# Performance work log

Hardware: AMD Instinct MI355X
Metric: run time of the kernel (lower is better)

## Reference

```python
import jax, jax.numpy as jnp
import numpy as np

EPS = 1e-5
SINKHORN_ITERS = 20
ALPHA_INIT = 0.01


def setup_inputs() -> dict:
    key = jax.random.key(0)
    ks = jax.random.split(key, 8)
    B, n, C = 8192, 4, 2048
    nC = n * C
    return {
        "x_expanded": jax.random.normal(ks[0], (B, n, C), dtype=jnp.float32),
        "rmsnorm_weight": jnp.ones((C,), dtype=jnp.float32),
        "phi_pre": 0.02 * jax.random.normal(ks[1], (n, nC), dtype=jnp.float32),
        "phi_post": 0.02 * jax.random.normal(ks[2], (n, nC), dtype=jnp.float32),
        "phi_res": 0.02 * jax.random.normal(ks[3], (n * n, nC), dtype=jnp.float32),
        "b_pre": jnp.zeros((n,), dtype=jnp.float32),
        "b_post": jnp.zeros((n,), dtype=jnp.float32),
        "b_res": jnp.zeros((n, n), dtype=jnp.float32),
        "alpha_pre": jnp.float32(ALPHA_INIT),
        "alpha_post": jnp.float32(ALPHA_INIT),
        "alpha_res": jnp.float32(ALPHA_INIT),
    }


def _rmsnorm(x, w, eps):
    # RMSNorm over the channel dim C of each stream
    ms = jnp.mean(x * x, axis=-1, keepdims=True)
    return x * jax.lax.rsqrt(ms + eps) * w


def _sinkhorn(logits, iters, eps):
    # logits: (B, n, n) -> doubly-stochastic matrix via Sinkhorn-Knopp
    m = jnp.exp(logits - jnp.max(logits, axis=(1, 2), keepdims=True))
    for _ in range(iters):
        m = m / (jnp.sum(m, axis=2, keepdims=True) + eps)  # row normalize
        m = m / (jnp.sum(m, axis=1, keepdims=True) + eps)  # col normalize
    return m


def reference(x_expanded, rmsnorm_weight, phi_pre, phi_post, phi_res,
              b_pre, b_post, b_res, alpha_pre, alpha_post, alpha_res):
    B, n, C = x_expanded.shape
    x_norm = _rmsnorm(x_expanded, rmsnorm_weight, EPS)   # (B, n, C)
    xf = x_norm.reshape(B, n * C)                         # (B, nC)

    # dynamic mixing coefficients from learned projections
    h_pre = alpha_pre * (xf @ phi_pre.T) + b_pre          # (B, n)
    h_post = alpha_post * (xf @ phi_post.T) + b_post      # (B, n)
    h_res_logits = (alpha_res * (xf @ phi_res.T) + b_res.reshape(-1)).reshape(B, n, n)

    h_res = _sinkhorn(h_res_logits, SINKHORN_ITERS, EPS)  # (B, n, n) doubly stochastic

    # blended mixing of the raw residual streams
    mixed = jnp.einsum('bij,bjc->bic', h_res, x_expanded)        # (B, n, C)
    agg = jnp.einsum('bn,bnc->bc', h_pre, x_expanded)            # (B, C)
    out = mixed + h_post[:, :, None] * agg[:, None, :]           # (B, n, C)
    return out
```

## Files before the change

kernel.cpp:

```cpp
#include <hip/hip_runtime.h>
#include <hip/hip_bf16.h>
#include <cstdint>

#define CH 2048
#define NCF 8192
#define NJ 24
#define RPB 4
#define EPS_F 1e-5f
#define SINK_ITERS 20

typedef float v4f __attribute__((ext_vector_type(4)));

__device__ __forceinline__ uint32_t bf16rne(float f) {
    uint32_t u = __float_as_uint(f);
    return (u + 0x7fffu + ((u >> 16) & 1u)) >> 16;
}

__device__ __forceinline__ float dot8(const uint4& x, const uint4& p, float acc) {
    asm("v_dot2_f32_bf16 %0, %1, %2, %0" : "+v"(acc) : "v"(x.x), "v"(p.x));
    asm("v_dot2_f32_bf16 %0, %1, %2, %0" : "+v"(acc) : "v"(x.y), "v"(p.y));
    asm("v_dot2_f32_bf16 %0, %1, %2, %0" : "+v"(acc) : "v"(x.z), "v"(p.z));
    asm("v_dot2_f32_bf16 %0, %1, %2, %0" : "+v"(acc) : "v"(x.w), "v"(p.w));
    return acc;
}

__global__ void __launch_bounds__(256) prep_phi_kernel(
    const float* __restrict__ w,
    const float* __restrict__ phi_pre,
    const float* __restrict__ phi_post,
    const float* __restrict__ phi_res,
    const float* __restrict__ alpha_pre,
    const float* __restrict__ alpha_post,
    const float* __restrict__ alpha_res,
    uint16_t* __restrict__ phiW)
{
    int idx = blockIdx.x * 256 + threadIdx.x;
    if (idx >= NJ * NCF) return;
    int j = idx / NCF;
    int k = idx - j * NCF;
    int c = k & (CH - 1);
    float v, a;
    if (j < 4)      { v = phi_pre[j * NCF + k];        a = alpha_pre[0]; }
    else if (j < 8) { v = phi_post[(j - 4) * NCF + k]; a = alpha_post[0]; }
    else            { v = phi_res[(j - 8) * NCF + k];  a = alpha_res[0]; }
    phiW[idx] = (uint16_t)bf16rne(v * a * w[c]);
}

__global__ void __launch_bounds__(512) mhc_main_kernel(
    const float* __restrict__ x,
    const uint16_t* __restrict__ phiW,
    const float* __restrict__ b_pre,
    const float* __restrict__ b_post,
    const float* __restrict__ b_res,
    float* __restrict__ out)
{
    const int t = threadIdx.x;
    const int lane = t & 63;
    const int wave = t >> 6;
    const long b0 = (long)blockIdx.x * RPB;

    __shared__ uint32_t xn[RPB][NCF / 2];
    __shared__ float4 red[RPB][8];
    __shared__ float H[RPB][24] __attribute__((aligned(16)));
    __shared__ float MS[RPB][16] __attribute__((aligned(16)));

    {
        const float4* xp = reinterpret_cast<const float4*>(x + b0 * NCF);
        #pragma unroll
        for (int rp = 0; rp < RPB; rp += 2) {
            float4 a[2][4];
            #pragma unroll
            for (int rr = 0; rr < 2; ++rr)
                #pragma unroll
                for (int jj = 0; jj < 4; ++jj)
                    a[rr][jj] = xp[(rp + rr) * 2048 + t + 512 * jj];

            float ss[2][4];
            #pragma unroll
            for (int rr = 0; rr < 2; ++rr) {
                const int r = rp + rr;
                #pragma unroll
                for (int jj = 0; jj < 4; ++jj) {
                    float4 v = a[rr][jj];
                    ss[rr][jj] = v.x*v.x + v.y*v.y + v.z*v.z + v.w*v.w;
                    *reinterpret_cast<uint2*>(&xn[r][2*t + 1024*jj]) =
                        make_uint2(bf16rne(v.x) | (bf16rne(v.y) << 16),
                                   bf16rne(v.z) | (bf16rne(v.w) << 16));
                }
            }
            #pragma unroll
            for (int m = 1; m < 64; m <<= 1) {
                #pragma unroll
                for (int rr = 0; rr < 2; ++rr)
                    #pragma unroll
                    for (int jj = 0; jj < 4; ++jj)
                        ss[rr][jj] += __shfl_xor(ss[rr][jj], m, 64);
            }
            if (lane == 0) {
                red[rp][wave]     = make_float4(ss[0][0], ss[0][1], ss[0][2], ss[0][3]);
                red[rp + 1][wave] = make_float4(ss[1][0], ss[1][1], ss[1][2], ss[1][3]);
            }
        }
    }
    __syncthreads();

    float scl[RPB][4];
    #pragma unroll
    for (int r = 0; r < RPB; ++r) {
        float sx = 0.f, sy = 0.f, sz = 0.f, sw = 0.f;
        #pragma unroll
        for (int w8 = 0; w8 < 8; ++w8) {
            float4 v = red[r][w8];
            sx += v.x; sy += v.y; sz += v.z; sw += v.w;
        }
        scl[r][0] = rsqrtf(sx * (1.0f / CH) + EPS_F);
        scl[r][1] = rsqrtf(sy * (1.0f / CH) + EPS_F);
        scl[r][2] = rsqrtf(sz * (1.0f / CH) + EPS_F);
        scl[r][3] = rsqrtf(sw * (1.0f / CH) + EPS_F);
    }

    float accT[3][RPB] = {};
    float accS[3][RPB] = {};
    {
        const uint16_t* pw = phiW + (size_t)(wave * 3) * NCF;
        const int kl = 8 * lane;
        const uint4* xr0 = reinterpret_cast<const uint4*>(xn[0]);
        const uint4* xr1 = reinterpret_cast<const uint4*>(xn[1]);
        const uint4* xr2 = reinterpret_cast<const uint4*>(xn[2]);
        const uint4* xr3 = reinterpret_cast<const uint4*>(xn[3]);

        uint4 pA0 = *reinterpret_cast<const uint4*>(pw + 0 * NCF + kl);
        uint4 pA1 = *reinterpret_cast<const uint4*>(pw + 1 * NCF + kl);
        uint4 pA2 = *reinterpret_cast<const uint4*>(pw + 2 * NCF + kl);
        uint4 xA0 = xr0[lane], xA1 = xr1[lane], xA2 = xr2[lane], xA3 = xr3[lane];

        #pragma unroll
        for (int u = 0; u < 16; u += 2) {
            const int iB = 64 * (u + 1) + lane;
            const int kB = 512 * (u + 1) + kl;
            uint4 pB0 = *reinterpret_cast<const uint4*>(pw + 0 * NCF + kB);
            uint4 pB1 = *reinterpret_cast<const uint4*>(pw + 1 * NCF + kB);
            uint4 pB2 = *reinterpret_cast<const uint4*>(pw + 2 * NCF + kB);
            uint4 xB0 = xr0[iB], xB1 = xr1[iB], xB2 = xr2[iB], xB3 = xr3[iB];

            accS[0][0] = dot8(xA0, pA0, accS[0][0]);
            accS[0][1] = dot8(xA1, pA0, accS[0][1]);
            accS[0][2] = dot8(xA2, pA0, accS[0][2]);
            accS[0][3] = dot8(xA3, pA0, accS[0][3]);
            accS[1][0] = dot8(xA0, pA1, accS[1][0]);
            accS[1][1] = dot8(xA1, pA1, accS[1][1]);
            accS[1][2] = dot8(xA2, pA1, accS[1][2]);
            accS[1][3] = dot8(xA3, pA1, accS[1][3]);
            accS[2][0] = dot8(xA0, pA2, accS[2][0]);
            accS[2][1] = dot8(xA1, pA2, accS[2][1]);
            accS[2][2] = dot8(xA2, pA2, accS[2][2]);
            accS[2][3] = dot8(xA3, pA2, accS[2][3]);

            if (u + 2 < 16) {
                const int iA = 64 * (u + 2) + lane;
                const int kA = 512 * (u + 2) + kl;
                pA0 = *reinterpret_cast<const uint4*>(pw + 0 * NCF + kA);
                pA1 = *reinterpret_cast<const uint4*>(pw + 1 * NCF + kA);
                pA2 = *reinterpret_cast<const uint4*>(pw + 2 * NCF + kA);
                xA0 = xr0[iA]; xA1 = xr1[iA]; xA2 = xr2[iA]; xA3 = xr3[iA];
            }

            accS[0][0] = dot8(xB0, pB0, accS[0][0]);
            accS[0][1] = dot8(xB1, pB0, accS[0][1]);
            accS[0][2] = dot8(xB2, pB0, accS[0][2]);
            accS[0][3] = dot8(xB3, pB0, accS[0][3]);
            accS[1][0] = dot8(xB0, pB1, accS[1][0]);
            accS[1][1] = dot8(xB1, pB1, accS[1][1]);
            accS[1][2] = dot8(xB2, pB1, accS[1][2]);
            accS[1][3] = dot8(xB3, pB1, accS[1][3]);
            accS[2][0] = dot8(xB0, pB2, accS[2][0]);
            accS[2][1] = dot8(xB1, pB2, accS[2][1]);
            accS[2][2] = dot8(xB2, pB2, accS[2][2]);
            accS[2][3] = dot8(xB3, pB2, accS[2][3]);

            if (((u + 1) & 3) == 3) {
                const int s = (u + 1) >> 2;
                #pragma unroll
                for (int jl = 0; jl < 3; ++jl) {
                    #pragma unroll
                    for (int r = 0; r < RPB; ++r) {
                        accT[jl][r] = fmaf(scl[r][s], accS[jl][r], accT[jl][r]);
                        accS[jl][r] = 0.f;
                    }
                }
            }
        }
    }
    {
        #pragma unroll
        for (int m = 1; m < 64; m <<= 1) {
            #pragma unroll
            for (int jl = 0; jl < 3; ++jl) {
                #pragma unroll
                for (int r = 0; r < RPB; ++r)
                    accT[jl][r] += __shfl_xor(accT[jl][r], m, 64);
            }
        }
        if (lane == 0) {
            #pragma unroll
            for (int jl = 0; jl < 3; ++jl) {
                int j = 3 * wave + jl;
                float bias;
                if (j < 4)      bias = b_pre[j];
                else if (j < 8) bias = b_post[j - 4];
                else            bias = b_res[j - 8];
                #pragma unroll
                for (int r = 0; r < RPB; ++r) H[r][j] = accT[jl][r] + bias;
            }
        }
    }
    __syncthreads();

    {
        const int r = lane >> 4;
        const int q = lane & 15;
        float L = H[r][8 + q];
        float mx = L;
        mx = fmaxf(mx, __shfl_xor(mx, 1, 64));
        mx = fmaxf(mx, __shfl_xor(mx, 2, 64));
        mx = fmaxf(mx, __shfl_xor(mx, 4, 64));
        mx = fmaxf(mx, __shfl_xor(mx, 8, 64));
        float m = __expf(L - mx);
        #pragma unroll
        for (int it = 0; it < SINK_ITERS; ++it) {
            float rs = m + __shfl_xor(m, 1, 64);
            rs += __shfl_xor(rs, 2, 64);
            m = m * __builtin_amdgcn_rcpf(rs + EPS_F);
            float cs = m + __shfl_xor(m, 4, 64);
            cs += __shfl_xor(cs, 8, 64);
            m = m * __builtin_amdgcn_rcpf(cs + EPS_F);
        }
        MS[r][q] = m;
    }

    #pragma unroll
    for (int r = 0; r < RPB; ++r) {
        const float4 hp = *reinterpret_cast<const float4*>(&H[r][0]);
        const float4 hq = *reinterpret_cast<const float4*>(&H[r][4]);
        float4 hrm[4];
        #pragma unroll
        for (int i = 0; i < 4; ++i)
            hrm[i] = *reinterpret_cast<const float4*>(&MS[r][4 * i]);
        float4 s[4];
        #pragma unroll
        for (int jj = 0; jj < 4; ++jj) {
            uint2 pk = *reinterpret_cast<const uint2*>(&xn[r][2 * t + 1024 * jj]);
            s[jj].x = __uint_as_float(pk.x << 16);
            s[jj].y = __uint_as_float(pk.x & 0xffff0000u);
            s[jj].z = __uint_as_float(pk.y << 16);
            s[jj].w = __uint_as_float(pk.y & 0xffff0000u);
        }
        float ax = hp.x*s[0].x + hp.y*s[1].x + hp.z*s[2].x + hp.w*s[3].x;
        float ay = hp.x*s[0].y + hp.y*s[1].y + hp.z*s[2].y + hp.w*s[3].y;
        float az = hp.x*s[0].z + hp.y*s[1].z + hp.z*s[2].z + hp.w*s[3].z;
        float aw = hp.x*s[0].w + hp.y*s[1].w + hp.z*s[2].w + hp.w*s[3].w;
        const float hqv[4] = {hq.x, hq.y, hq.z, hq.w};
        v4f* op = reinterpret_cast<v4f*>(out + (b0 + r) * NCF + 4 * t);
        #pragma unroll
        for (int i = 0; i < 4; ++i) {
            v4f o;
            o.x = hrm[i].x*s[0].x + hrm[i].y*s[1].x + hrm[i].z*s[2].x + hrm[i].w*s[3].x + hqv[i]*ax;
            o.y = hrm[i].x*s[0].y + hrm[i].y*s[1].y + hrm[i].z*s[2].y + hrm[i].w*s[3].y + hqv[i]*ay;
            o.z = hrm[i].x*s[0].z + hrm[i].y*s[1].z + hrm[i].z*s[2].z + hrm[i].w*s[3].z + hqv[i]*az;
            o.w = hrm[i].x*s[0].w + hrm[i].y*s[1].w + hrm[i].z*s[2].w + hrm[i].w*s[3].w + hqv[i]*aw;
            __builtin_nontemporal_store(o, op + i * 512);
        }
    }
}

extern "C" void kernel_launch(void* const* d_in, const int* in_sizes, int n_in,
                              void* d_out, int out_size, void* d_ws, size_t ws_size,
                              hipStream_t stream)
{
    const float* x        = (const float*)d_in[0];
    const float* w        = (const float*)d_in[1];
    const float* phi_pre  = (const float*)d_in[2];
    const float* phi_post = (const float*)d_in[3];
    const float* phi_res  = (const float*)d_in[4];
    const float* b_pre    = (const float*)d_in[5];
    const float* b_post   = (const float*)d_in[6];
    const float* b_res    = (const float*)d_in[7];
    const float* a_pre    = (const float*)d_in[8];
    const float* a_post   = (const float*)d_in[9];
    const float* a_res    = (const float*)d_in[10];
    float* out = (float*)d_out;
    uint16_t* phiW = (uint16_t*)d_ws;

    const int B = in_sizes[0] / NCF;

    prep_phi_kernel<<<(NJ * NCF + 255) / 256, 256, 0, stream>>>(
        w, phi_pre, phi_post, phi_res, a_pre, a_post, a_res, phiW);

    mhc_main_kernel<<<B / RPB, 512, 0, stream>>>(
        x, phiW, b_pre, b_post, b_res, out);
}
```

Before: 133.1 us.

## Split fused kernel into coefficient kernel and fp32 mixing kernel

```diff
diff --git a/kernel.cpp b/kernel.cpp
--- a/kernel.cpp
+++ b/kernel.cpp
@@ -14,6 +14,12 @@
 __device__ __forceinline__ uint32_t bf16rne(float f) {
     uint32_t u = __float_as_uint(f);
     return (u + 0x7fffu + ((u >> 16) & 1u)) >> 16;
+}
+
+__device__ __forceinline__ uint32_t cvtpk(float lo, float hi) {
+    uint32_t r;
+    asm("v_cvt_pk_bf16_f32 %0, %1, %2" : "=v"(r) : "v"(lo), "v"(hi));
+    return r;
 }
 
 __device__ __forceinline__ float dot8(const uint4& x, const uint4& p, float acc) {
@@ -46,13 +52,13 @@
     phiW[idx] = (uint16_t)bf16rne(v * a * w[c]);
 }
 
-__global__ void __launch_bounds__(512) mhc_main_kernel(
+__global__ void __launch_bounds__(512) h_kernel(
     const float* __restrict__ x,
     const uint16_t* __restrict__ phiW,
     const float* __restrict__ b_pre,
     const float* __restrict__ b_post,
     const float* __restrict__ b_res,
-    float* __restrict__ out)
+    float* __restrict__ hbuf)
 {
     const int t = threadIdx.x;
     const int lane = t & 63;
@@ -84,8 +90,7 @@
                     float4 v = a[rr][jj];
                     ss[rr][jj] = v.x*v.x + v.y*v.y + v.z*v.z + v.w*v.w;
                     *reinterpret_cast<uint2*>(&xn[r][2*t + 1024*jj]) =
-                        make_uint2(bf16rne(v.x) | (bf16rne(v.y) << 16),
-                                   bf16rne(v.z) | (bf16rne(v.w) << 16));
+                        make_uint2(cvtpk(v.x, v.y), cvtpk(v.z, v.w));
                 }
             }
             #pragma unroll
@@ -238,38 +243,67 @@
         MS[r][q] = m;
     }
 
-    #pragma unroll
-    for (int r = 0; r < RPB; ++r) {
-        const float4 hp = *reinterpret_cast<const float4*>(&H[r][0]);
-        const float4 hq = *reinterpret_cast<const float4*>(&H[r][4]);
-        float4 hrm[4];
-        #pragma unroll
-        for (int i = 0; i < 4; ++i)
-            hrm[i] = *reinterpret_cast<const float4*>(&MS[r][4 * i]);
-        float4 s[4];
-        #pragma unroll
-        for (int jj = 0; jj < 4; ++jj) {
-            uint2 pk = *reinterpret_cast<const uint2*>(&xn[r][2 * t + 1024 * jj]);
-            s[jj].x = __uint_as_float(pk.x << 16);
-            s[jj].y = __uint_as_float(pk.x & 0xffff0000u);
-            s[jj].z = __uint_as_float(pk.y << 16);
-            s[jj].w = __uint_as_float(pk.y & 0xffff0000u);
-        }
-        float ax = hp.x*s[0].x + hp.y*s[1].x + hp.z*s[2].x + hp.w*s[3].x;
-        float ay = hp.x*s[0].y + hp.y*s[1].y + hp.z*s[2].y + hp.w*s[3].y;
-        float az = hp.x*s[0].z + hp.y*s[1].z + hp.z*s[2].z + hp.w*s[3].z;
-        float aw = hp.x*s[0].w + hp.y*s[1].w + hp.z*s[2].w + hp.w*s[3].w;
-        const float hqv[4] = {hq.x, hq.y, hq.z, hq.w};
-        v4f* op = reinterpret_cast<v4f*>(out + (b0 + r) * NCF + 4 * t);
-        #pragma unroll
-        for (int i = 0; i < 4; ++i) {
-            v4f o;
-            o.x = hrm[i].x*s[0].x + hrm[i].y*s[1].x + hrm[i].z*s[2].x + hrm[i].w*s[3].x + hqv[i]*ax;
-            o.y = hrm[i].x*s[0].y + hrm[i].y*s[1].y + hrm[i].z*s[2].y + hrm[i].w*s[3].y + hqv[i]*ay;
-            o.z = hrm[i].x*s[0].z + hrm[i].y*s[1].z + hrm[i].z*s[2].z + hrm[i].w*s[3].z + hqv[i]*az;
-            o.w = hrm[i].x*s[0].w + hrm[i].y*s[1].w + hrm[i].z*s[2].w + hrm[i].w*s[3].w + hqv[i]*aw;
-            __builtin_nontemporal_store(o, op + i * 512);
-        }
+    if (t < 96) {
+        const int r = t / 24;
+        const int k = t - 24 * r;
+        float v = (k < 8) ? H[r][k] : MS[r][k - 8];
+        hbuf[(b0 + r) * 24 + k] = v;
+    }
+}
+
+__global__ void __launch_bounds__(512) mix_kernel(
+    const float* __restrict__ x,
+    const float* __restrict__ hbuf,
+    float* __restrict__ out)
+{
+    const int t = threadIdx.x;
+    const long b = blockIdx.x;
+
+    const float4* hb = reinterpret_cast<const float4*>(hbuf + b * 24);
+    const float4 hp = hb[0];
+    const float4 hq = hb[1];
+    const float4 h0 = hb[2], h1 = hb[3], h2 = hb[4], h3 = hb[5];
+
+    const float4* xp = reinterpret_cast<const float4*>(x + b * NCF) + t;
+    const float4 s0 = xp[0], s1 = xp[512], s2 = xp[1024], s3 = xp[1536];
+
+    const float ax = hp.x*s0.x + hp.y*s1.x + hp.z*s2.x + hp.w*s3.x;
+    const float ay = hp.x*s0.y + hp.y*s1.y + hp.z*s2.y + hp.w*s3.y;
+    const float az = hp.x*s0.z + hp.y*s1.z + hp.z*s2.z + hp.w*s3.z;
+    const float aw = hp.x*s0.w + hp.y*s1.w + hp.z*s2.w + hp.w*s3.w;
+
+    v4f* op = reinterpret_cast<v4f*>(out + b * NCF) + t;
+    {
+        v4f o;
+        o.x = h0.x*s0.x + h0.y*s1.x + h0.z*s2.x + h0.w*s3.x + hq.x*ax;
+        o.y = h0.x*s0.y + h0.y*s1.y + h0.z*s2.y + h0.w*s3.y + hq.x*ay;
+        o.z = h0.x*s0.z + h0.y*s1.z + h0.z*s2.z + h0.w*s3.z + hq.x*az;
+        o.w = h0.x*s0.w + h0.y*s1.w + h0.z*s2.w + h0.w*s3.w + hq.x*aw;
+        __builtin_nontemporal_store(o, op);
+    }
+    {
+        v4f o;
+        o.x = h1.x*s0.x + h1.y*s1.x + h1.z*s2.x + h1.w*s3.x + hq.y*ax;
+        o.y = h1.x*s0.y + h1.y*s1.y + h1.z*s2.y + h1.w*s3.y + hq.y*ay;
+        o.z = h1.x*s0.z + h1.y*s1.z + h1.z*s2.z + h1.w*s3.z + hq.y*az;
+        o.w = h1.x*s0.w + h1.y*s1.w + h1.z*s2.w + h1.w*s3.w + hq.y*aw;
+        __builtin_nontemporal_store(o, op + 512);
+    }
+    {
+        v4f o;
+        o.x = h2.x*s0.x + h2.y*s1.x + h2.z*s2.x + h2.w*s3.x + hq.z*ax;
+        o.y = h2.x*s0.y + h2.y*s1.y + h2.z*s2.y + h2.w*s3.y + hq.z*ay;
+        o.z = h2.x*s0.z + h2.y*s1.z + h2.z*s2.z + h2.w*s3.z + hq.z*az;
+        o.w = h2.x*s0.w + h2.y*s1.w + h2.z*s2.w + h2.w*s3.w + hq.z*aw;
+        __builtin_nontemporal_store(o, op + 1024);
+    }
+    {
+        v4f o;
+        o.x = h3.x*s0.x + h3.y*s1.x + h3.z*s2.x + h3.w*s3.x + hq.w*ax;
+        o.y = h3.x*s0.y + h3.y*s1.y + h3.z*s2.y + h3.w*s3.y + hq.w*ay;
+        o.z = h3.x*s0.z + h3.y*s1.z + h3.z*s2.z + h3.w*s3.z + hq.w*az;
+        o.w = h3.x*s0.w + h3.y*s1.w + h3.z*s2.w + h3.w*s3.w + hq.w*aw;
+        __builtin_nontemporal_store(o, op + 1536);
     }
 }
 
@@ -289,13 +323,17 @@
     const float* a_post   = (const float*)d_in[9];
     const float* a_res    = (const float*)d_in[10];
     float* out = (float*)d_out;
+
     uint16_t* phiW = (uint16_t*)d_ws;
+    float* hbuf = (float*)((char*)d_ws + (size_t)NJ * NCF * 2);
 
     const int B = in_sizes[0] / NCF;
 
     prep_phi_kernel<<<(NJ * NCF + 255) / 256, 256, 0, stream>>>(
         w, phi_pre, phi_post, phi_res, a_pre, a_post, a_res, phiW);
 
-    mhc_main_kernel<<<B / RPB, 512, 0, stream>>>(
-        x, phiW, b_pre, b_post, b_res, out);
-}
+    h_kernel<<<B / RPB, 512, 0, stream>>>(
+        x, phiW, b_pre, b_post, b_res, hbuf);
+
+    mix_kernel<<<B, 512, 0, stream>>>(x, hbuf, out);
+}
```

Result: slower. 172.0 us (+29.2%).

## Make main kernel persistent with register prefetch of next row group

Applied to the files above, without the earlier changes.

```diff
diff --git a/kernel.cpp b/kernel.cpp
--- a/kernel.cpp
+++ b/kernel.cpp
@@ -6,6 +6,7 @@
 #define NCF 8192
 #define NJ 24
 #define RPB 4
+#define NBLK 512
 #define EPS_F 1e-5f
 #define SINK_ITERS 20
 
@@ -14,6 +15,12 @@
 __device__ __forceinline__ uint32_t bf16rne(float f) {
     uint32_t u = __float_as_uint(f);
     return (u + 0x7fffu + ((u >> 16) & 1u)) >> 16;
+}
+
+__device__ __forceinline__ uint32_t cvtpk(float lo, float hi) {
+    uint32_t r;
+    asm("v_cvt_pk_bf16_f32 %0, %1, %2" : "=v"(r) : "v"(lo), "v"(hi));
+    return r;
 }
 
 __device__ __forceinline__ float dot8(const uint4& x, const uint4& p, float acc) {
@@ -46,230 +53,244 @@
     phiW[idx] = (uint16_t)bf16rne(v * a * w[c]);
 }
 
-__global__ void __launch_bounds__(512) mhc_main_kernel(
+__global__ void __launch_bounds__(512, 2) mhc_main_kernel(
     const float* __restrict__ x,
     const uint16_t* __restrict__ phiW,
     const float* __restrict__ b_pre,
     const float* __restrict__ b_post,
     const float* __restrict__ b_res,
-    float* __restrict__ out)
+    float* __restrict__ out,
+    int ngroups)
 {
     const int t = threadIdx.x;
     const int lane = t & 63;
     const int wave = t >> 6;
-    const long b0 = (long)blockIdx.x * RPB;
 
     __shared__ uint32_t xn[RPB][NCF / 2];
     __shared__ float4 red[RPB][8];
     __shared__ float H[RPB][24] __attribute__((aligned(16)));
     __shared__ float MS[RPB][16] __attribute__((aligned(16)));
 
+    float bias[3];
+    #pragma unroll
+    for (int jl = 0; jl < 3; ++jl) {
+        int j = 3 * wave + jl;
+        bias[jl] = (j < 4) ? b_pre[j] : (j < 8) ? b_post[j - 4] : b_res[j - 8];
+    }
+
+    const float4* x4 = reinterpret_cast<const float4*>(x);
+
+    float4 xr[16];
     {
-        const float4* xp = reinterpret_cast<const float4*>(x + b0 * NCF);
+        const float4* xp = x4 + (long)blockIdx.x * RPB * 2048;
         #pragma unroll
-        for (int rp = 0; rp < RPB; rp += 2) {
-            float4 a[2][4];
-            #pragma unroll
-            for (int rr = 0; rr < 2; ++rr)
-                #pragma unroll
-                for (int jj = 0; jj < 4; ++jj)
-                    a[rr][jj] = xp[(rp + rr) * 2048 + t + 512 * jj];
-
-            float ss[2][4];
-            #pragma unroll
-            for (int rr = 0; rr < 2; ++rr) {
-                const int r = rp + rr;
+        for (int r = 0; r < RPB; ++r)
+            #pragma unroll
+            for (int jj = 0; jj < 4; ++jj)
+                xr[r * 4 + jj] = xp[r * 2048 + t + 512 * jj];
+    }
+
+    #pragma unroll 1
+    for (long g = blockIdx.x; g < ngroups; g += NBLK) {
+        const long b0 = g * RPB;
+
+        {
+            float ssv[16];
+            #pragma unroll
+            for (int r = 0; r < RPB; ++r) {
                 #pragma unroll
                 for (int jj = 0; jj < 4; ++jj) {
-                    float4 v = a[rr][jj];
-                    ss[rr][jj] = v.x*v.x + v.y*v.y + v.z*v.z + v.w*v.w;
+                    float4 v = xr[r * 4 + jj];
+                    ssv[r * 4 + jj] = v.x*v.x + v.y*v.y + v.z*v.z + v.w*v.w;
                     *reinterpret_cast<uint2*>(&xn[r][2*t + 1024*jj]) =
-                        make_uint2(bf16rne(v.x) | (bf16rne(v.y) << 16),
-                                   bf16rne(v.z) | (bf16rne(v.w) << 16));
+                        make_uint2(cvtpk(v.x, v.y), cvtpk(v.z, v.w));
                 }
             }
             #pragma unroll
-            for (int m = 1; m < 64; m <<= 1) {
-                #pragma unroll
-                for (int rr = 0; rr < 2; ++rr)
+            for (int m = 1; m < 64; m <<= 1)
+                #pragma unroll
+                for (int i = 0; i < 16; ++i)
+                    ssv[i] += __shfl_xor(ssv[i], m, 64);
+            if (lane == 0) {
+                #pragma unroll
+                for (int r = 0; r < RPB; ++r)
+                    red[r][wave] = make_float4(ssv[r*4], ssv[r*4+1], ssv[r*4+2], ssv[r*4+3]);
+            }
+        }
+        __syncthreads();
+
+        float scl[RPB][4];
+        #pragma unroll
+        for (int r = 0; r < RPB; ++r) {
+            float sx = 0.f, sy = 0.f, sz = 0.f, sw = 0.f;
+            #pragma unroll
+            for (int w8 = 0; w8 < 8; ++w8) {
+                float4 v = red[r][w8];
+                sx += v.x; sy += v.y; sz += v.z; sw += v.w;
+            }
+            scl[r][0] = rsqrtf(sx * (1.0f / CH) + EPS_F);
+            scl[r][1] = rsqrtf(sy * (1.0f / CH) + EPS_F);
+            scl[r][2] = rsqrtf(sz * (1.0f / CH) + EPS_F);
+            scl[r][3] = rsqrtf(sw * (1.0f / CH) + EPS_F);
+        }
+
+        float accT[3][RPB] = {};
+        float accS[3][RPB] = {};
+        {
+            const uint16_t* pw = phiW + (size_t)(wave * 3) * NCF;
+            const int kl = 8 * lane;
+            const uint4* xr0 = reinterpret_cast<const uint4*>(xn[0]);
+            const uint4* xr1 = reinterpret_cast<const uint4*>(xn[1]);
+            const uint4* xr2 = reinterpret_cast<const uint4*>(xn[2]);
+            const uint4* xr3 = reinterpret_cast<const uint4*>(xn[3]);
+
+            uint4 pA0 = *reinterpret_cast<const uint4*>(pw + 0 * NCF + kl);
+            uint4 pA1 = *reinterpret_cast<const uint4*>(pw + 1 * NCF + kl);
+            uint4 pA2 = *reinterpret_cast<const uint4*>(pw + 2 * NCF + kl);
+            uint4 xA0 = xr0[lane], xA1 = xr1[lane], xA2 = xr2[lane], xA3 = xr3[lane];
+
+            #pragma unroll
+            for (int u = 0; u < 16; u += 2) {
+                const int iB = 64 * (u + 1) + lane;
+                const int kB = 512 * (u + 1) + kl;
+                uint4 pB0 = *reinterpret_cast<const uint4*>(pw + 0 * NCF + kB);
+                uint4 pB1 = *reinterpret_cast<const uint4*>(pw + 1 * NCF + kB);
+                uint4 pB2 = *reinterpret_cast<const uint4*>(pw + 2 * NCF + kB);
+                uint4 xB0 = xr0[iB], xB1 = xr1[iB], xB2 = xr2[iB], xB3 = xr3[iB];
+
+                accS[0][0] = dot8(xA0, pA0, accS[0][0]);
+                accS[0][1] = dot8(xA1, pA0, accS[0][1]);
+                accS[0][2] = dot8(xA2, pA0, accS[0][2]);
+                accS[0][3] = dot8(xA3, pA0, accS[0][3]);
+                accS[1][0] = dot8(xA0, pA1, accS[1][0]);
+                accS[1][1] = dot8(xA1, pA1, accS[1][1]);
+                accS[1][2] = dot8(xA2, pA1, accS[1][2]);
+                accS[1][3] = dot8(xA3, pA1, accS[1][3]);
+                accS[2][0] = dot8(xA0, pA2, accS[2][0]);
+                accS[2][1] = dot8(xA1, pA2, accS[2][1]);
+                accS[2][2] = dot8(xA2, pA2, accS[2][2]);
+                accS[2][3] = dot8(xA3, pA2, accS[2][3]);
+
+                if (u + 2 < 16) {
+                    const int iA = 64 * (u + 2) + lane;
+                    const int kA = 512 * (u + 2) + kl;
+                    pA0 = *reinterpret_cast<const uint4*>(pw + 0 * NCF + kA);
+                    pA1 = *reinterpret_cast<const uint4*>(pw + 1 * NCF + kA);
+                    pA2 = *reinterpret_cast<const uint4*>(pw + 2 * NCF + kA);
+                    xA0 = xr0[iA]; xA1 = xr1[iA]; xA2 = xr2[iA]; xA3 = xr3[iA];
+                }
+
+                accS[0][0] = dot8(xB0, pB0, accS[0][0]);
+                accS[0][1] = dot8(xB1, pB0, accS[0][1]);
+                accS[0][2] = dot8(xB2, pB0, accS[0][2]);
+                accS[0][3] = dot8(xB3, pB0, accS[0][3]);
+                accS[1][0] = dot8(xB0, pB1, accS[1][0]);
+                accS[1][1] = dot8(xB1, pB1, accS[1][1]);
+                accS[1][2] = dot8(xB2, pB1, accS[1][2]);
+                accS[1][3] = dot8(xB3, pB1, accS[1][3]);
+                accS[2][0] = dot8(xB0, pB2, accS[2][0]);
+                accS[2][1] = dot8(xB1, pB2, accS[2][1]);
+                accS[2][2] = dot8(xB2, pB2, accS[2][2]);
+                accS[2][3] = dot8(xB3, pB2, accS[2][3]);
+
+                if (((u + 1) & 3) == 3) {
+                    const int s = (u + 1) >> 2;
                     #pragma unroll
-                    for (int jj = 0; jj < 4; ++jj)
-                        ss[rr][jj] += __shfl_xor(ss[rr][jj], m, 64);
-            }
-            if (lane == 0) {
-                red[rp][wave]     = make_float4(ss[0][0], ss[0][1], ss[0][2], ss[0][3]);
-                red[rp + 1][wave] = make_float4(ss[1][0], ss[1][1], ss[1][2], ss[1][3]);
-            }
-        }
-    }
-    __syncthreads();
-
-    float scl[RPB][4];
-    #pragma unroll
-    for (int r = 0; r < RPB; ++r) {
-        float sx = 0.f, sy = 0.f, sz = 0.f, sw = 0.f;
-        #pragma unroll
-        for (int w8 = 0; w8 < 8; ++w8) {
-            float4 v = red[r][w8];
-            sx += v.x; sy += v.y; sz += v.z; sw += v.w;
-        }
-        scl[r][0] = rsqrtf(sx * (1.0f / CH) + EPS_F);
-        scl[r][1] = rsqrtf(sy * (1.0f / CH) + EPS_F);
-        scl[r][2] = rsqrtf(sz * (1.0f / CH) + EPS_F);
-        scl[r][3] = rsqrtf(sw * (1.0f / CH) + EPS_F);
-    }
-
-    float accT[3][RPB] = {};
-    float accS[3][RPB] = {};
-    {
-        const uint16_t* pw = phiW + (size_t)(wave * 3) * NCF;
-        const int kl = 8 * lane;
-        const uint4* xr0 = reinterpret_cast<const uint4*>(xn[0]);
-        const uint4* xr1 = reinterpret_cast<const uint4*>(xn[1]);
-        const uint4* xr2 = reinterpret_cast<const uint4*>(xn[2]);
-        const uint4* xr3 = reinterpret_cast<const uint4*>(xn[3]);
-
-        uint4 pA0 = *reinterpret_cast<const uint4*>(pw + 0 * NCF + kl);
-        uint4 pA1 = *reinterpret_cast<const uint4*>(pw + 1 * NCF + kl);
-        uint4 pA2 = *reinterpret_cast<const uint4*>(pw + 2 * NCF + kl);
-        uint4 xA0 = xr0[lane], xA1 = xr1[lane], xA2 = xr2[lane], xA3 = xr3[lane];
-
-        #pragma unroll
-        for (int u = 0; u < 16; u += 2) {
-            const int iB = 64 * (u + 1) + lane;
-            const int kB = 512 * (u + 1) + kl;
-            uint4 pB0 = *reinterpret_cast<const uint4*>(pw + 0 * NCF + kB);
-            uint4 pB1 = *reinterpret_cast<const uint4*>(pw + 1 * NCF + kB);
-            uint4 pB2 = *reinterpret_cast<const uint4*>(pw + 2 * NCF + kB);
-            uint4 xB0 = xr0[iB], xB1 = xr1[iB], xB2 = xr2[iB], xB3 = xr3[iB];
-
-            accS[0][0] = dot8(xA0, pA0, accS[0][0]);
-            accS[0][1] = dot8(xA1, pA0, accS[0][1]);
-            accS[0][2] = dot8(xA2, pA0, accS[0][2]);
-            accS[0][3] = dot8(xA3, pA0, accS[0][3]);
-            accS[1][0] = dot8(xA0, pA1, accS[1][0]);
-            accS[1][1] = dot8(xA1, pA1, accS[1][1]);
-            accS[1][2] = dot8(xA2, pA1, accS[1][2]);
-            accS[1][3] = dot8(xA3, pA1, accS[1][3]);
-            accS[2][0] = dot8(xA0, pA2, accS[2][0]);
-            accS[2][1] = dot8(xA1, pA2, accS[2][1]);
-            accS[2][2] = dot8(xA2, pA2, accS[2][2]);
-            accS[2][3] = dot8(xA3, pA2, accS[2][3]);
-
-            if (u + 2 < 16) {
-                const int iA = 64 * (u + 2) + lane;
-                const int kA = 512 * (u + 2) + kl;
-                pA0 = *reinterpret_cast<const uint4*>(pw + 0 * NCF + kA);
-                pA1 = *reinterpret_cast<const uint4*>(pw + 1 * NCF + kA);
-                pA2 = *reinterpret_cast<const uint4*>(pw + 2 * NCF + kA);
-                xA0 = xr0[iA]; xA1 = xr1[iA]; xA2 = xr2[iA]; xA3 = xr3[iA];
-            }
-
-            accS[0][0] = dot8(xB0, pB0, accS[0][0]);
-            accS[0][1] = dot8(xB1, pB0, accS[0][1]);
-            accS[0][2] = dot8(xB2, pB0, accS[0][2]);
-            accS[0][3] = dot8(xB3, pB0, accS[0][3]);
-            accS[1][0] = dot8(xB0, pB1, accS[1][0]);
-            accS[1][1] = dot8(xB1, pB1, accS[1][1]);
-            accS[1][2] = dot8(xB2, pB1, accS[1][2]);
-            accS[1][3] = dot8(xB3, pB1, accS[1][3]);
-            accS[2][0] = dot8(xB0, pB2, accS[2][0]);
-            accS[2][1] = dot8(xB1, pB2, accS[2][1]);
-            accS[2][2] = dot8(xB2, pB2, accS[2][2]);
-            accS[2][3] = dot8(xB3, pB2, accS[2][3]);
-
-            if (((u + 1) & 3) == 3) {
-                const int s = (u + 1) >> 2;
-                #pragma unroll
-                for (int jl = 0; jl < 3; ++jl) {
-                    #pragma unroll
-                    for (int r = 0; r < RPB; ++r) {
-                        accT[jl][r] = fmaf(scl[r][s], accS[jl][r], accT[jl][r]);
-                        accS[jl][r] = 0.f;
+                    for (int jl = 0; jl < 3; ++jl) {
+                        #pragma unroll
+                        for (int r = 0; r < RPB; ++r) {
+                            accT[jl][r] = fmaf(scl[r][s], accS[jl][r], accT[jl][r]);
+                            accS[jl][r] = 0.f;
+                        }
                     }
                 }
             }
         }
-    }
-    {
+
+        if (g + NBLK < ngroups) {
+            const float4* xp = x4 + (g + NBLK) * RPB * 2048;
+            #pragma unroll
+            for (int r = 0; r < RPB; ++r)
+                #pragma unroll
+                for (int jj = 0; jj < 4; ++jj)
+                    xr[r * 4 + jj] = xp[r * 2048 + t + 512 * jj];
+        }
+
+        {
+            #pragma unroll
+            for (int m = 1; m < 64; m <<= 1) {
+                #pragma unroll
+                for (int jl = 0; jl < 3; ++jl)
+                    #pragma unroll
+                    for (int r = 0; r < RPB; ++r)
+                        accT[jl][r] += __shfl_xor(accT[jl][r], m, 64);
+            }
+            if (lane == 0) {
+                #pragma unroll
+                for (int jl = 0; jl < 3; ++jl)
+                    #pragma unroll
+                    for (int r = 0; r < RPB; ++r)
+                        H[r][3 * wave + jl] = accT[jl][r] + bias[jl];
+            }
+        }
+        __syncthreads();
+
+        {
+            const int r = lane >> 4;
+            const int q = lane & 15;
+            float L = H[r][8 + q];
+            float mx = L;
+            mx = fmaxf(mx, __shfl_xor(mx, 1, 64));
+            mx = fmaxf(mx, __shfl_xor(mx, 2, 64));
+            mx = fmaxf(mx, __shfl_xor(mx, 4, 64));
+            mx = fmaxf(mx, __shfl_xor(mx, 8, 64));
+            float m = __expf(L - mx);
+            #pragma unroll
+            for (int it = 0; it < SINK_ITERS; ++it) {
+                float rs = m + __shfl_xor(m, 1, 64);
+                rs += __shfl_xor(rs, 2, 64);
+                m = m * __builtin_amdgcn_rcpf(rs + EPS_F);
+                float cs = m + __shfl_xor(m, 4, 64);
+                cs += __shfl_xor(cs, 8, 64);
+                m = m * __builtin_amdgcn_rcpf(cs + EPS_F);
+            }
+            MS[r][q] = m;
+        }
+
         #pragma unroll
-        for (int m = 1; m < 64; m <<= 1) {
-            #pragma unroll
-            for (int jl = 0; jl < 3; ++jl) {
-                #pragma unroll
-                for (int r = 0; r < RPB; ++r)
-                    accT[jl][r] += __shfl_xor(accT[jl][r], m, 64);
-            }
-        }
-        if (lane == 0) {
-            #pragma unroll
-            for (int jl = 0; jl < 3; ++jl) {
-                int j = 3 * wave + jl;
-                float bias;
-                if (j < 4)      bias = b_pre[j];
-                else if (j < 8) bias = b_post[j - 4];
-                else            bias = b_res[j - 8];
-                #pragma unroll
-                for (int r = 0; r < RPB; ++r) H[r][j] = accT[jl][r] + bias;
-            }
-        }
-    }
-    __syncthreads();
-
-    {
-        const int r = lane >> 4;
-        const int q = lane & 15;
-        float L = H[r][8 + q];
-        float mx = L;
-        mx = fmaxf(mx, __shfl_xor(mx, 1, 64));
-        mx = fmaxf(mx, __shfl_xor(mx, 2, 64));
-        mx = fmaxf(mx, __shfl_xor(mx, 4, 64));
-        mx = fmaxf(mx, __shfl_xor(mx, 8, 64));
-        float m = __expf(L - mx);
-        #pragma unroll
-        for (int it = 0; it < SINK_ITERS; ++it) {
-            float rs = m + __shfl_xor(m, 1, 64);
-            rs += __shfl_xor(rs, 2, 64);
-            m = m * __builtin_amdgcn_rcpf(rs + EPS_F);
-            float cs = m + __shfl_xor(m, 4, 64);
-            cs += __shfl_xor(cs, 8, 64);
-            m = m * __builtin_amdgcn_rcpf(cs + EPS_F);
-        }
-        MS[r][q] = m;
-    }
-
-    #pragma unroll
-    for (int r = 0; r < RPB; ++r) {
-        const float4 hp = *reinterpret_cast<const float4*>(&H[r][0]);
-        const float4 hq = *reinterpret_cast<const float4*>(&H[r][4]);
-        float4 hrm[4];
-        #pragma unroll
-        for (int i = 0; i < 4; ++i)
-            hrm[i] = *reinterpret_cast<const float4*>(&MS[r][4 * i]);
-        float4 s[4];
-        #pragma unroll
-        for (int jj = 0; jj < 4; ++jj) {
-            uint2 pk = *reinterpret_cast<const uint2*>(&xn[r][2 * t + 1024 * jj]);
-            s[jj].x = __uint_as_float(pk.x << 16);
-            s[jj].y = __uint_as_float(pk.x & 0xffff0000u);
-            s[jj].z = __uint_as_float(pk.y << 16);
-            s[jj].w = __uint_as_float(pk.y & 0xffff0000u);
-        }
-        float ax = hp.x*s[0].x + hp.y*s[1].x + hp.z*s[2].x + hp.w*s[3].x;
-        float ay = hp.x*s[0].y + hp.y*s[1].y + hp.z*s[2].y + hp.w*s[3].y;
-        float az = hp.x*s[0].z + hp.y*s[1].z + hp.z*s[2].z + hp.w*s[3].z;
-        float aw = hp.x*s[0].w + hp.y*s[1].w + hp.z*s[2].w + hp.w*s[3].w;
-        const float hqv[4] = {hq.x, hq.y, hq.z, hq.w};
-        v4f* op = reinterpret_cast<v4f*>(out + (b0 + r) * NCF + 4 * t);
-        #pragma unroll
-        for (int i = 0; i < 4; ++i) {
-            v4f o;
-            o.x = hrm[i].x*s[0].x + hrm[i].y*s[1].x + hrm[i].z*s[2].x + hrm[i].w*s[3].x + hqv[i]*ax;
-            o.y = hrm[i].x*s[0].y + hrm[i].y*s[1].y + hrm[i].z*s[2].y + hrm[i].w*s[3].y + hqv[i]*ay;
-            o.z = hrm[i].x*s[0].z + hrm[i].y*s[1].z + hrm[i].z*s[2].z + hrm[i].w*s[3].z + hqv[i]*az;
-            o.w = hrm[i].x*s[0].w + hrm[i].y*s[1].w + hrm[i].z*s[2].w + hrm[i].w*s[3].w + hqv[i]*aw;
-            __builtin_nontemporal_store(o, op + i * 512);
-        }
+        for (int r = 0; r < RPB; ++r) {
+            const float4 hp = *reinterpret_cast<const float4*>(&H[r][0]);
+            const float4 hq = *reinterpret_cast<const float4*>(&H[r][4]);
+            float4 hrm[4];
+            #pragma unroll
+            for (int i = 0; i < 4; ++i)
+                hrm[i] = *reinterpret_cast<const float4*>(&MS[r][4 * i]);
+            float4 s[4];
+            #pragma unroll
+            for (int jj = 0; jj < 4; ++jj) {
+                uint2 pk = *reinterpret_cast<const uint2*>(&xn[r][2 * t + 1024 * jj]);
+                s[jj].x = __uint_as_float(pk.x << 16);
+                s[jj].y = __uint_as_float(pk.x & 0xffff0000u);
+                s[jj].z = __uint_as_float(pk.y << 16);
+                s[jj].w = __uint_as_float(pk.y & 0xffff0000u);
+            }
+            float ax = hp.x*s[0].x + hp.y*s[1].x + hp.z*s[2].x + hp.w*s[3].x;
+            float ay = hp.x*s[0].y + hp.y*s[1].y + hp.z*s[2].y + hp.w*s[3].y;
+            float az = hp.x*s[0].z + hp.y*s[1].z + hp.z*s[2].z + hp.w*s[3].z;
+            float aw = hp.x*s[0].w + hp.y*s[1].w + hp.z*s[2].w + hp.w*s[3].w;
+            const float hqv[4] = {hq.x, hq.y, hq.z, hq.w};
+            v4f* op = reinterpret_cast<v4f*>(out + (b0 + r) * NCF + 4 * t);
+            #pragma unroll
+            for (int i = 0; i < 4; ++i) {
+                v4f o;
+                o.x = hrm[i].x*s[0].x + hrm[i].y*s[1].x + hrm[i].z*s[2].x + hrm[i].w*s[3].x + hqv[i]*ax;
+                o.y = hrm[i].x*s[0].y + hrm[i].y*s[1].y + hrm[i].z*s[2].y + hrm[i].w*s[3].y + hqv[i]*ay;
+                o.z = hrm[i].x*s[0].z + hrm[i].y*s[1].z + hrm[i].z*s[2].z + hrm[i].w*s[3].z + hqv[i]*az;
+                o.w = hrm[i].x*s[0].w + hrm[i].y*s[1].w + hrm[i].w*s[3].w + hrm[i].z*s[2].w + hqv[i]*aw;
+                __builtin_nontemporal_store(o, op + i * 512);
+            }
+        }
+        __syncthreads();
     }
 }
 
@@ -292,10 +313,11 @@
     uint16_t* phiW = (uint16_t*)d_ws;
 
     const int B = in_sizes[0] / NCF;
+    const int ngroups = B / RPB;
 
     prep_phi_kernel<<<(NJ * NCF + 255) / 256, 256, 0, stream>>>(
         w, phi_pre, phi_post, phi_res, a_pre, a_post, a_res, phiW);
 
-    mhc_main_kernel<<<B / RPB, 512, 0, stream>>>(
-        x, phiW, b_pre, b_post, b_res, out);
-}
+    mhc_main_kernel<<<NBLK, 512, 0, stream>>>(
+        x, phiW, b_pre, b_post, b_res, out, ngroups);
+}
```

Measured after the change: 235.3 us. 76.7% more time.

## Fold post/pre outer product into mixing matrix, hardware bf16 pack, batch x loads

Applied to the files above, without the earlier changes.

```diff
diff --git a/kernel.cpp b/kernel.cpp
--- a/kernel.cpp
+++ b/kernel.cpp
@@ -14,6 +14,12 @@
 __device__ __forceinline__ uint32_t bf16rne(float f) {
     uint32_t u = __float_as_uint(f);
     return (u + 0x7fffu + ((u >> 16) & 1u)) >> 16;
+}
+
+__device__ __forceinline__ uint32_t cvtpk(float lo, float hi) {
+    uint32_t r;
+    asm("v_cvt_pk_bf16_f32 %0, %1, %2" : "=v"(r) : "v"(lo), "v"(hi));
+    return r;
 }
 
 __device__ __forceinline__ float dot8(const uint4& x, const uint4& p, float acc) {
@@ -66,40 +72,36 @@
 
     {
         const float4* xp = reinterpret_cast<const float4*>(x + b0 * NCF);
-        #pragma unroll
-        for (int rp = 0; rp < RPB; rp += 2) {
-            float4 a[2][4];
-            #pragma unroll
-            for (int rr = 0; rr < 2; ++rr)
+        float4 a[RPB][4];
+        #pragma unroll
+        for (int r = 0; r < RPB; ++r)
+            #pragma unroll
+            for (int jj = 0; jj < 4; ++jj)
+                a[r][jj] = xp[r * 2048 + t + 512 * jj];
+
+        float ss[RPB][4];
+        #pragma unroll
+        for (int r = 0; r < RPB; ++r) {
+            #pragma unroll
+            for (int jj = 0; jj < 4; ++jj) {
+                float4 v = a[r][jj];
+                ss[r][jj] = v.x*v.x + v.y*v.y + v.z*v.z + v.w*v.w;
+                *reinterpret_cast<uint2*>(&xn[r][2*t + 1024*jj]) =
+                    make_uint2(cvtpk(v.x, v.y), cvtpk(v.z, v.w));
+            }
+        }
+        #pragma unroll
+        for (int m = 1; m < 64; m <<= 1) {
+            #pragma unroll
+            for (int r = 0; r < RPB; ++r)
                 #pragma unroll
                 for (int jj = 0; jj < 4; ++jj)
-                    a[rr][jj] = xp[(rp + rr) * 2048 + t + 512 * jj];
-
-            float ss[2][4];
-            #pragma unroll
-            for (int rr = 0; rr < 2; ++rr) {
-                const int r = rp + rr;
-                #pragma unroll
-                for (int jj = 0; jj < 4; ++jj) {
-                    float4 v = a[rr][jj];
-                    ss[rr][jj] = v.x*v.x + v.y*v.y + v.z*v.z + v.w*v.w;
-                    *reinterpret_cast<uint2*>(&xn[r][2*t + 1024*jj]) =
-                        make_uint2(bf16rne(v.x) | (bf16rne(v.y) << 16),
-                                   bf16rne(v.z) | (bf16rne(v.w) << 16));
-                }
-            }
-            #pragma unroll
-            for (int m = 1; m < 64; m <<= 1) {
-                #pragma unroll
-                for (int rr = 0; rr < 2; ++rr)
-                    #pragma unroll
-                    for (int jj = 0; jj < 4; ++jj)
-                        ss[rr][jj] += __shfl_xor(ss[rr][jj], m, 64);
-            }
-            if (lane == 0) {
-                red[rp][wave]     = make_float4(ss[0][0], ss[0][1], ss[0][2], ss[0][3]);
-                red[rp + 1][wave] = make_float4(ss[1][0], ss[1][1], ss[1][2], ss[1][3]);
-            }
+                    ss[r][jj] += __shfl_xor(ss[r][jj], m, 64);
+        }
+        if (lane == 0) {
+            #pragma unroll
+            for (int r = 0; r < RPB; ++r)
+                red[r][wave] = make_float4(ss[r][0], ss[r][1], ss[r][2], ss[r][3]);
         }
     }
     __syncthreads();
@@ -242,10 +244,16 @@
     for (int r = 0; r < RPB; ++r) {
         const float4 hp = *reinterpret_cast<const float4*>(&H[r][0]);
         const float4 hq = *reinterpret_cast<const float4*>(&H[r][4]);
-        float4 hrm[4];
-        #pragma unroll
-        for (int i = 0; i < 4; ++i)
-            hrm[i] = *reinterpret_cast<const float4*>(&MS[r][4 * i]);
+        float4 M[4];
+        #pragma unroll
+        for (int i = 0; i < 4; ++i) {
+            float4 hrm = *reinterpret_cast<const float4*>(&MS[r][4 * i]);
+            const float q = (i == 0) ? hq.x : (i == 1) ? hq.y : (i == 2) ? hq.z : hq.w;
+            M[i].x = fmaf(q, hp.x, hrm.x);
+            M[i].y = fmaf(q, hp.y, hrm.y);
+            M[i].z = fmaf(q, hp.z, hrm.z);
+            M[i].w = fmaf(q, hp.w, hrm.w);
+        }
         float4 s[4];
         #pragma unroll
         for (int jj = 0; jj < 4; ++jj) {
@@ -255,19 +263,14 @@
             s[jj].z = __uint_as_float(pk.y << 16);
             s[jj].w = __uint_as_float(pk.y & 0xffff0000u);
         }
-        float ax = hp.x*s[0].x + hp.y*s[1].x + hp.z*s[2].x + hp.w*s[3].x;
-        float ay = hp.x*s[0].y + hp.y*s[1].y + hp.z*s[2].y + hp.w*s[3].y;
-        float az = hp.x*s[0].z + hp.y*s[1].z + hp.z*s[2].z + hp.w*s[3].z;
-        float aw = hp.x*s[0].w + hp.y*s[1].w + hp.z*s[2].w + hp.w*s[3].w;
-        const float hqv[4] = {hq.x, hq.y, hq.z, hq.w};
         v4f* op = reinterpret_cast<v4f*>(out + (b0 + r) * NCF + 4 * t);
         #pragma unroll
         for (int i = 0; i < 4; ++i) {
             v4f o;
-            o.x = hrm[i].x*s[0].x + hrm[i].y*s[1].x + hrm[i].z*s[2].x + hrm[i].w*s[3].x + hqv[i]*ax;
-            o.y = hrm[i].x*s[0].y + hrm[i].y*s[1].y + hrm[i].z*s[2].y + hrm[i].w*s[3].y + hqv[i]*ay;
-            o.z = hrm[i].x*s[0].z + hrm[i].y*s[1].z + hrm[i].z*s[2].z + hrm[i].w*s[3].z + hqv[i]*az;
-            o.w = hrm[i].x*s[0].w + hrm[i].y*s[1].w + hrm[i].z*s[2].w + hrm[i].w*s[3].w + hqv[i]*aw;
+            o.x = M[i].x*s[0].x + M[i].y*s[1].x + M[i].z*s[2].x + M[i].w*s[3].x;
+            o.y = M[i].x*s[0].y + M[i].y*s[1].y + M[i].z*s[2].y + M[i].w*s[3].y;
+            o.z = M[i].x*s[0].z + M[i].y*s[1].z + M[i].z*s[2].z + M[i].w*s[3].z;
+            o.w = M[i].x*s[0].w + M[i].y*s[1].w + M[i].z*s[2].w + M[i].w*s[3].w;
             __builtin_nontemporal_store(o, op + i * 512);
         }
     }
```

New measurement: 135.0 us. No clear change (+1.4%).
